# Kernel tuning notes

Measured on AMD Instinct MI355X. Metric: run time of the kernel, lower is better.

## Reference

```python
import jax, jax.numpy as jnp
import numpy as np

D_MODEL = 1024
N_HEADS = 16
D_K = D_MODEL // N_HEADS
D_FF = 4096
EPS = 1e-6


def setup_inputs() -> dict:
    key = jax.random.key(0)
    ks = jax.random.split(key, 12)
    s = 1.0 / np.sqrt(D_MODEL)
    inp = {
        "x": jax.random.normal(ks[0], (4, 2048, D_MODEL), jnp.float32),
        "src_mask": jnp.ones((4, 1, 1, 2048), jnp.int32),
        "Wq": jax.random.normal(ks[1], (D_MODEL, D_MODEL), jnp.float32) * s,
        "bq": jnp.zeros((D_MODEL,), jnp.float32),
        "Wk": jax.random.normal(ks[2], (D_MODEL, D_MODEL), jnp.float32) * s,
        "bk": jnp.zeros((D_MODEL,), jnp.float32),
        "Wv": jax.random.normal(ks[3], (D_MODEL, D_MODEL), jnp.float32) * s,
        "bv": jnp.zeros((D_MODEL,), jnp.float32),
        "Wo": jax.random.normal(ks[4], (D_MODEL, D_MODEL), jnp.float32) * s,
        "bo": jnp.zeros((D_MODEL,), jnp.float32),
        "W1": jax.random.normal(ks[5], (D_MODEL, D_FF), jnp.float32) * s,
        "b1": jnp.zeros((D_FF,), jnp.float32),
        "W2": jax.random.normal(ks[6], (D_FF, D_MODEL), jnp.float32) * (1.0 / np.sqrt(D_FF)),
        "b2": jnp.zeros((D_MODEL,), jnp.float32),
        # scalar LayerNormalization params (alpha=ones(1), bias=zeros(1)) for the 2 residual norms
        "ln1_alpha": jnp.ones((1,), jnp.float32),
        "ln1_bias": jnp.zeros((1,), jnp.float32),
        "ln2_alpha": jnp.ones((1,), jnp.float32),
        "ln2_bias": jnp.zeros((1,), jnp.float32),
    }
    return inp


def _layernorm(x, alpha, bias):
    # matches torch: mean + std (unbiased, ddof=1), (x-mean)/(std+eps)
    mean = jnp.mean(x, axis=-1, keepdims=True)
    std = jnp.std(x, axis=-1, keepdims=True, ddof=1)
    return alpha * ((x - mean) / (std + EPS)) + bias


def _mha(x, mask, Wq, bq, Wk, bk, Wv, bv, Wo, bo):
    B, S, _ = x.shape
    q = (x @ Wq + bq).reshape(B, S, N_HEADS, D_K).transpose(0, 2, 1, 3)
    k = (x @ Wk + bk).reshape(B, S, N_HEADS, D_K).transpose(0, 2, 1, 3)
    v = (x @ Wv + bv).reshape(B, S, N_HEADS, D_K).transpose(0, 2, 1, 3)
    scores = jnp.einsum("bhqd,bhkd->bhqk", q, k) / jnp.sqrt(jnp.float32(D_K))
    scores = jnp.where(mask == 0, jnp.float32(-1e9), scores)
    attn = jax.nn.softmax(scores, axis=-1)
    ctx = jnp.einsum("bhqk,bhkd->bhqd", attn, v)
    ctx = ctx.transpose(0, 2, 1, 3).reshape(B, S, D_MODEL)
    return ctx @ Wo + bo


def reference(x, src_mask, Wq, bq, Wk, bk, Wv, bv, Wo, bo, W1, b1, W2, b2,
              ln1_alpha, ln1_bias, ln2_alpha, ln2_bias):
    # pre-norm residual 1: self-attention
    h = _layernorm(x, ln1_alpha, ln1_bias)
    x = x + _mha(h, src_mask, Wq, bq, Wk, bk, Wv, bv, Wo, bo)
    # pre-norm residual 2: FFN
    h = _layernorm(x, ln2_alpha, ln2_bias)
    ff = jax.nn.relu(h @ W1 + b1) @ W2 + b2
    return x + ff
```

## Files before the change

### kernel.cpp

```cpp
#include <hip/hip_runtime.h>

typedef __attribute__((ext_vector_type(8))) short v8s;
typedef __attribute__((ext_vector_type(8))) unsigned short v8u;
typedef __attribute__((ext_vector_type(4))) unsigned short v4u;
typedef __attribute__((ext_vector_type(4))) float f32x4;

#define DEV __device__ __forceinline__

DEV unsigned short f2bf(float f) {
  union { float f; unsigned u; } v; v.f = f;
  unsigned r = v.u + 0x7fffu + ((v.u >> 16) & 1u);
  return (unsigned short)(r >> 16);
}

DEV float fexp2(float x) {
  float r; asm("v_exp_f32 %0, %1" : "=v"(r) : "v"(x)); return r;
}

DEV void gload16(const unsigned short* g, unsigned short* l) {
  __builtin_amdgcn_global_load_lds(
      (const __attribute__((address_space(1))) unsigned int*)g,
      (__attribute__((address_space(3))) unsigned int*)l, 16, 0, 0);
}

#define SL2E 0.1803368801111204f

__global__ __launch_bounds__(256) void ln_kernel(
    const float* __restrict__ x, unsigned short* __restrict__ h,
    const float* __restrict__ alpha, const float* __restrict__ beta)
{
  int row = blockIdx.x;
  int tid = threadIdx.x;
  const float4* xr = reinterpret_cast<const float4*>(x + (size_t)row * 1024);
  float4 v = xr[tid];
  float s  = v.x + v.y + v.z + v.w;
  float ss = v.x * v.x + v.y * v.y + v.z * v.z + v.w * v.w;
#pragma unroll
  for (int off = 1; off < 64; off <<= 1) {
    s  += __shfl_xor(s, off);
    ss += __shfl_xor(ss, off);
  }
  __shared__ float ps[4][2];
  int wid = tid >> 6, lane = tid & 63;
  if (lane == 0) { ps[wid][0] = s; ps[wid][1] = ss; }
  __syncthreads();
  s  = ps[0][0] + ps[1][0] + ps[2][0] + ps[3][0];
  ss = ps[0][1] + ps[1][1] + ps[2][1] + ps[3][1];
  float mean = s * (1.0f / 1024.0f);
  float var  = (ss - 1024.0f * mean * mean) * (1.0f / 1023.0f);
  float inv  = 1.0f / (sqrtf(fmaxf(var, 0.0f)) + 1e-6f);
  float a = alpha[0], b = beta[0];
  v4u o;
  o[0] = f2bf(a * ((v.x - mean) * inv) + b);
  o[1] = f2bf(a * ((v.y - mean) * inv) + b);
  o[2] = f2bf(a * ((v.z - mean) * inv) + b);
  o[3] = f2bf(a * ((v.w - mean) * inv) + b);
  *reinterpret_cast<v4u*>(h + (size_t)row * 1024 + tid * 4) = o;
}

__global__ __launch_bounds__(256) void transpose_convert(
    const float* __restrict__ W, unsigned short* __restrict__ Wt, int K, int N)
{
  __shared__ float t[32][33];
  int n0 = blockIdx.x * 32, k0 = blockIdx.y * 32;
  int tx = threadIdx.x, ty = threadIdx.y;
#pragma unroll
  for (int i = 0; i < 4; ++i)
    t[ty + i * 8][tx] = W[(size_t)(k0 + ty + i * 8) * N + n0 + tx];
  __syncthreads();
#pragma unroll
  for (int i = 0; i < 4; ++i)
    Wt[(size_t)(n0 + ty + i * 8) * K + k0 + tx] = f2bf(t[tx][ty + i * 8]);
}

enum { MODE_QKV = 0, MODE_RES = 2, MODE_FFN1 = 3 };

template <int MODE>
__global__ __launch_bounds__(512, 1) void gemm_256(
    const unsigned short* __restrict__ A, const unsigned short* __restrict__ Bt,
    const float* __restrict__ bias0, const float* __restrict__ bias1,
    const float* __restrict__ bias2,
    void* __restrict__ o0, void* __restrict__ o1, void* __restrict__ o2,
    int M, int N, int K)
{
  __shared__ unsigned short lds[2][512 * 64];

  int nbx = M >> 8, nwg = gridDim.x;
  int lin = blockIdx.x;
  int qq = nwg >> 3, rr = nwg & 7;
  int xcd = lin & 7, idx = lin >> 3;
  int swz = (xcd < rr ? xcd * (qq + 1) : rr * (qq + 1) + (xcd - rr) * qq) + idx;
  int bx = swz % nbx, by = swz / nbx;

  int tid = threadIdx.x, lane = tid & 63, wid = tid >> 6;
  int wm = wid >> 2, wn = wid & 3;
  int g = lane >> 4, c0 = lane & 15;
  int rowBase = bx * 256, colBase = by * 256;

  const unsigned short* Ab = A  + (size_t)rowBase * K;
  const unsigned short* Bb = Bt + (size_t)colBase * K;
  int NT = K >> 6;

  const unsigned short* src[8]; int dq[8];
#pragma unroll
  for (int i = 0; i < 8; ++i) {
    int q = i * 512 + tid;
    dq[i] = q;
    if (i < 4) {
      int r = q >> 3, p = q & 7;
      src[i] = Ab + (size_t)r * K + 8 * (p ^ (r & 7));
    } else {
      int qb2 = q - 2048, r = qb2 >> 3, p = qb2 & 7;
      src[i] = Bb + (size_t)r * K + 8 * (p ^ (r & 7));
    }
  }

  f32x4 acc[8][4];
#pragma unroll
  for (int m = 0; m < 8; ++m)
#pragma unroll
    for (int n = 0; n < 4; ++n) acc[m][n] = (f32x4){0.f, 0.f, 0.f, 0.f};

#define STG256(tt) do { \
    unsigned short* sb_ = &lds[(tt) & 1][0]; int ko_ = (tt) << 6; \
    _Pragma("unroll") for (int i = 0; i < 8; ++i) gload16(src[i] + ko_, sb_ + dq[i] * 8); \
  } while (0)

  STG256(0);
  asm volatile("s_waitcnt vmcnt(0)" ::: "memory");
  __builtin_amdgcn_s_barrier();
  asm volatile("" ::: "memory");

  for (int t = 0; t < NT; ++t) {
    const char* buf = (const char*)&lds[t & 1][0];
    bool more = (t + 1 < NT);
    if (more) STG256(t + 1);
    int e = (c0 & 7) << 4;

#pragma unroll
    for (int ph = 0; ph < 2; ++ph) {
      v8s af[8], bfr[4];
#pragma unroll
      for (int m = 0; m < 8; ++m) {
        int row = wm * 128 + m * 16 + c0;
        af[m] = *reinterpret_cast<const v8s*>(
            buf + row * 128 + ((ph * 64 + g * 16) ^ e));
      }
#pragma unroll
      for (int n = 0; n < 4; ++n) {
        int row = wn * 64 + n * 16 + c0;
        bfr[n] = *reinterpret_cast<const v8s*>(
            buf + 32768 + row * 128 + ((ph * 64 + g * 16) ^ e));
      }

      __builtin_amdgcn_s_setprio(1);
#pragma unroll
      for (int m = 0; m < 8; ++m)
#pragma unroll
        for (int n = 0; n < 4; ++n)
          acc[m][n] = __builtin_amdgcn_mfma_f32_16x16x32_bf16(
              af[m], bfr[n], acc[m][n], 0, 0, 0);
      __builtin_amdgcn_s_setprio(0);
    }

    if (more) asm volatile("s_waitcnt vmcnt(0)" ::: "memory");
    __builtin_amdgcn_sched_barrier(0);
    __builtin_amdgcn_s_barrier();
    asm volatile("" ::: "memory");
  }
#undef STG256

#pragma unroll
  for (int mf = 0; mf < 8; ++mf) {
#pragma unroll
    for (int nf = 0; nf < 4; ++nf) {
#pragma unroll
      for (int r = 0; r < 4; ++r) {
        int row = rowBase + wm * 128 + mf * 16 + g * 4 + r;
        int col = colBase + wn * 64 + nf * 16 + c0;
        float v = acc[mf][nf][r];
        if constexpr (MODE == MODE_QKV) {
          int sect = colBase >> 10;
          int cs = col & 1023;
          const float* bp = sect == 0 ? bias0 : (sect == 1 ? bias1 : bias2);
          v += bp[cs];
          int hh = cs >> 6, d = cs & 63;
          int b = row >> 11, sI = row & 2047;
          size_t bh = (size_t)(b * 16 + hh);
          if (sect == 0) {
            ((unsigned short*)o0)[(bh * 2048 + sI) * 64 + d] = f2bf(v * SL2E);
          } else if (sect == 1) {
            ((unsigned short*)o1)[(bh * 2048 + sI) * 64 + d] = f2bf(v);
          } else {
            int k6 = sI & 63;
            int slot = ((k6 >> 5) << 5) | (((k6 >> 2) & 3) << 3) |
                       (((k6 >> 4) & 1) << 2) | (k6 & 3);
            int e2 = slot ^ ((d & 7) << 3);
            ((unsigned short*)o2)[((bh * 32 + (sI >> 6)) * 64 + d) * 64 + e2] = f2bf(v);
          }
        } else {
          v += bias0[col];
          ((unsigned short*)o0)[(size_t)row * N + col] = f2bf(fmaxf(v, 0.0f));
        }
      }
    }
  }
}

#define BUF_ELEMS ((128 + 256) * 64)

DEV void stage_part(const unsigned short* Aptr, const unsigned short* Bptr,
                    unsigned short* buf, int K, int part, int wid, int lane)
{
  {
    int d = (part * 8 + wid) * 64 + lane;
    int r = d >> 3, p = d & 7;
    gload16(Aptr + (size_t)r * K + 8 * (p ^ (r & 7)),
            buf + (size_t)(part * 8 + wid) * 512);
  }
#pragma unroll
  for (int j = 0; j < 2; ++j) {
    int ib = part * 2 + j;
    int d = (ib * 8 + wid) * 64 + lane;
    int r = d >> 3, p = d & 7;
    gload16(Bptr + (size_t)r * K + 8 * (p ^ (r & 7)),
            buf + 128 * 64 + (size_t)(ib * 8 + wid) * 512);
  }
}

__global__ __launch_bounds__(512, 2) void gemm_pipe_res(
    const unsigned short* __restrict__ A, const unsigned short* __restrict__ Bt,
    const float* __restrict__ bias0, const float* __restrict__ resid,
    float* __restrict__ o0, int M, int N, int K)
{
  __shared__ unsigned short lds[3 * BUF_ELEMS];

  int nbx = M >> 7, nwg = gridDim.x;
  int lin = blockIdx.x;
  int qq = nwg >> 3, rr = nwg & 7;
  int xcd = lin & 7, idx = lin >> 3;
  int swz = (xcd < rr ? xcd * (qq + 1) : rr * (qq + 1) + (xcd - rr) * qq) + idx;
  int bx = swz % nbx, by = swz / nbx;

  int tid = threadIdx.x, lane = tid & 63, wid = tid >> 6;
  int wm = wid >> 2, wn = wid & 3;
  int g = lane >> 4, c0 = lane & 15;
  int rowBase = bx * 128, colBase = by * 256;

  const unsigned short* Ab = A  + (size_t)rowBase * K;
  const unsigned short* Bb = Bt + (size_t)colBase * K;
  int NT = K >> 6;

  f32x4 acc[4][4];
#pragma unroll
  for (int m = 0; m < 4; ++m)
#pragma unroll
    for (int n = 0; n < 4; ++n) acc[m][n] = (f32x4){0.f, 0.f, 0.f, 0.f};

  stage_part(Ab, Bb, lds, K, 0, wid, lane);
  stage_part(Ab, Bb, lds, K, 1, wid, lane);
  stage_part(Ab + 64, Bb + 64, lds + BUF_ELEMS, K, 0, wid, lane);
  stage_part(Ab + 64, Bb + 64, lds + BUF_ELEMS, K, 1, wid, lane);
  asm volatile("s_waitcnt vmcnt(6)" ::: "memory");
  __builtin_amdgcn_s_barrier();
  asm volatile("" ::: "memory");

  int cur = 0;
  for (int t = 0; t < NT; ++t) {
    const char* Abuf = (const char*)(lds + cur * BUF_ELEMS);
    const char* Bbuf = Abuf + 128 * 128;
    int nxt2 = cur + 2; if (nxt2 >= 3) nxt2 -= 3;
    unsigned short* sbuf = lds + nxt2 * BUF_ELEMS;
    bool doStage = (t + 2 < NT);
    int ks_ = (t + 2) << 6;
    int e = (c0 & 7) << 4;

#pragma unroll
    for (int ph = 0; ph < 2; ++ph) {
      v8s af[4], bfr[4];
#pragma unroll
      for (int m = 0; m < 4; ++m)
        af[m] = *reinterpret_cast<const v8s*>(
            Abuf + (wm * 64 + m * 16 + c0) * 128 + ((ph * 64 + g * 16) ^ e));
#pragma unroll
      for (int n = 0; n < 4; ++n)
        bfr[n] = *reinterpret_cast<const v8s*>(
            Bbuf + (wn * 64 + n * 16 + c0) * 128 + ((ph * 64 + g * 16) ^ e));

      if (doStage) stage_part(Ab + ks_, Bb + ks_, sbuf, K, ph, wid, lane);

      __builtin_amdgcn_s_setprio(1);
#pragma unroll
      for (int m = 0; m < 4; ++m)
#pragma unroll
        for (int n = 0; n < 4; ++n)
          acc[m][n] = __builtin_amdgcn_mfma_f32_16x16x32_bf16(
              af[m], bfr[n], acc[m][n], 0, 0, 0);
      __builtin_amdgcn_s_setprio(0);
    }

    if (doStage)            asm volatile("s_waitcnt vmcnt(6)" ::: "memory");
    else if (t + 1 < NT)    asm volatile("s_waitcnt vmcnt(0)" ::: "memory");
    __builtin_amdgcn_sched_barrier(0);
    __builtin_amdgcn_s_barrier();
    asm volatile("" ::: "memory");
    cur = cur + 1; if (cur >= 3) cur -= 3;
  }

#pragma unroll
  for (int mf = 0; mf < 4; ++mf) {
#pragma unroll
    for (int nf = 0; nf < 4; ++nf) {
#pragma unroll
      for (int r = 0; r < 4; ++r) {
        int row = rowBase + wm * 64 + mf * 16 + g * 4 + r;
        int col = colBase + wn * 64 + nf * 16 + c0;
        float v = acc[mf][nf][r] + bias0[col];
        o0[(size_t)row * N + col] = resid[(size_t)row * N + col] + v;
      }
    }
  }
}

__global__ __launch_bounds__(256) void attn_kernel(
    const unsigned short* __restrict__ q, const unsigned short* __restrict__ k,
    const unsigned short* __restrict__ vP, const int* __restrict__ mask,
    unsigned short* __restrict__ ctx)
{
  const int S = 2048, DK = 64, NT = 32;
  int bh = blockIdx.x;
  int b = bh >> 4, hh = bh & 15;
  int qbase = blockIdx.y * 128;
  int tid = threadIdx.x, lane = tid & 63, wid = tid >> 6;
  int g = lane >> 4, c0 = lane & 15;

  __shared__ unsigned short Ks[3 * 4096];
  __shared__ unsigned short Vs[3 * 4096];
  __shared__ unsigned short Mb[2048];

  const unsigned short* qb  = q  + (size_t)bh * S * DK;
  const unsigned short* kb  = k  + (size_t)bh * S * DK;
  const unsigned short* vPb = vP + (size_t)bh * 32 * 4096;
  const int* mb = mask + b * S;

  const int4* mb4 = reinterpret_cast<const int4*>(mb);
  int4 ma = mb4[tid * 2], mc = mb4[tid * 2 + 1];
  unsigned short bneg = f2bf(-1e9f);
  v8u bw;
  bw[0] = ma.x ? 0 : bneg; bw[1] = ma.y ? 0 : bneg;
  bw[2] = ma.z ? 0 : bneg; bw[3] = ma.w ? 0 : bneg;
  bw[4] = mc.x ? 0 : bneg; bw[5] = mc.y ? 0 : bneg;
  bw[6] = mc.z ? 0 : bneg; bw[7] = mc.w ? 0 : bneg;
  *reinterpret_cast<v8u*>(&Mb[tid * 8]) = bw;
  int ok = (ma.x && ma.y && ma.z && ma.w && mc.x && mc.y && mc.z && mc.w) ? 1 : 0;
  int allValid = __syncthreads_and(ok);

  int qrow = qbase + wid * 32 + c0;
  v8s aq[2][2];
#pragma unroll
  for (int s = 0; s < 2; ++s)
#pragma unroll
    for (int t = 0; t < 2; ++t)
      aq[s][t] = *reinterpret_cast<const v8s*>(
          &qb[(size_t)(qrow + s * 16) * DK + t * 32 + g * 8]);

  int i0 = tid, i1 = tid + 256;
  int r0 = i0 >> 3, m0 = i0 & 7;
  int r1 = i1 >> 3, m1 = i1 & 7;
  int ko0 = r0 * DK + 8 * (m0 ^ (r0 & 7));
  int ko1 = r1 * DK + 8 * (m1 ^ (r1 & 7));

  f32x4 acc[2][4];
#pragma unroll
  for (int s = 0; s < 2; ++s)
#pragma unroll
    for (int no = 0; no < 4; ++no) acc[s][no] = (f32x4){0.f, 0.f, 0.f, 0.f};
  float lsum0 = 0.f, lsum1 = 0.f;

#define ASTAGE(bi, tt) do { \
    int tb_ = (tt) * 4096; \
    gload16(kb + tb_ + ko0, Ks + (bi) * 4096 + i0 * 8); \
    gload16(kb + tb_ + ko1, Ks + (bi) * 4096 + i1 * 8); \
    gload16(vPb + tb_ + i0 * 8, Vs + (bi) * 4096 + i0 * 8); \
    gload16(vPb + tb_ + i1 * 8, Vs + (bi) * 4096 + i1 * 8); \
  } while (0)

  ASTAGE(0, 0);
  ASTAGE(1, 1);
  asm volatile("s_waitcnt vmcnt(4)" ::: "memory");
  __builtin_amdgcn_s_barrier();
  asm volatile("" ::: "memory");

  int cur = 0, nx2 = 2;
  for (int t = 0; t < NT; ++t) {
    bool more2 = (t + 2 < NT);
    if (more2) ASTAGE(nx2, t + 2);
    const unsigned short* Kc = Ks + cur * 4096;
    const unsigned short* Vc = Vs + cur * 4096;

    float p0[16], p1[16];
#pragma unroll
    for (int n = 0; n < 4; ++n) {
      int kvr = n * 16 + c0;
      const char* krow = (const char*)(Kc + kvr * DK);
      int sw = (kvr & 7) << 4;
      v8s ak0 = *reinterpret_cast<const v8s*>(krow + ((g * 16) ^ sw));
      v8s ak1 = *reinterpret_cast<const v8s*>(krow + ((64 + g * 16) ^ sw));
      f32x4 s0 = (f32x4){0.f, 0.f, 0.f, 0.f};
      f32x4 s1 = (f32x4){0.f, 0.f, 0.f, 0.f};
      s0 = __builtin_amdgcn_mfma_f32_16x16x32_bf16(ak0, aq[0][0], s0, 0, 0, 0);
      s0 = __builtin_amdgcn_mfma_f32_16x16x32_bf16(ak1, aq[0][1], s0, 0, 0, 0);
      s1 = __builtin_amdgcn_mfma_f32_16x16x32_bf16(ak0, aq[1][0], s1, 0, 0, 0);
      s1 = __builtin_amdgcn_mfma_f32_16x16x32_bf16(ak1, aq[1][1], s1, 0, 0, 0);
#pragma unroll
      for (int r = 0; r < 4; ++r) { p0[n * 4 + r] = s0[r]; p1[n * 4 + r] = s1[r]; }
    }
    if (!allValid) {
#pragma unroll
      for (int n = 0; n < 4; ++n) {
        v4u mbv = *reinterpret_cast<const v4u*>(&Mb[t * 64 + n * 16 + g * 4]);
#pragma unroll
        for (int r = 0; r < 4; ++r) {
          union { unsigned u; float f; } cv; cv.u = ((unsigned)mbv[r]) << 16;
          p0[n * 4 + r] += cv.f; p1[n * 4 + r] += cv.f;
        }
      }
    }

    float ts0 = 0.f, ts1 = 0.f;
#pragma unroll
    for (int i = 0; i < 16; ++i) {
      p0[i] = fexp2(p0[i]); ts0 += p0[i];
      p1[i] = fexp2(p1[i]); ts1 += p1[i];
    }
    lsum0 += ts0; lsum1 += ts1;

    v8s pb0[2], pb1[2];
#pragma unroll
    for (int c = 0; c < 2; ++c) {
      union { v8s s; unsigned u[4]; } k0, k1;
#pragma unroll
      for (int hp = 0; hp < 4; ++hp) {
        asm("v_cvt_pk_bf16_f32 %0, %1, %2"
            : "=v"(k0.u[hp]) : "v"(p0[c * 8 + 2 * hp]), "v"(p0[c * 8 + 2 * hp + 1]));
        asm("v_cvt_pk_bf16_f32 %0, %1, %2"
            : "=v"(k1.u[hp]) : "v"(p1[c * 8 + 2 * hp]), "v"(p1[c * 8 + 2 * hp + 1]));
      }
      pb0[c] = k0.s; pb1[c] = k1.s;
    }

#pragma unroll
    for (int c = 0; c < 2; ++c) {
#pragma unroll
      for (int no = 0; no < 4; ++no) {
        int d = no * 16 + c0;
        v8s av = *reinterpret_cast<const v8s*>(
            (const char*)(Vc + d * 64) + ((c * 64 + g * 16) ^ ((d & 7) << 4)));
        acc[0][no] = __builtin_amdgcn_mfma_f32_16x16x32_bf16(av, pb0[c], acc[0][no], 0, 0, 0);
        acc[1][no] = __builtin_amdgcn_mfma_f32_16x16x32_bf16(av, pb1[c], acc[1][no], 0, 0, 0);
      }
    }

    if (more2)              asm volatile("s_waitcnt vmcnt(4)" ::: "memory");
    else if (t + 1 < NT)    asm volatile("s_waitcnt vmcnt(0)" ::: "memory");
    __builtin_amdgcn_sched_barrier(0);
    __builtin_amdgcn_s_barrier();
    asm volatile("" ::: "memory");
    cur = (cur + 1 < 3) ? cur + 1 : 0;
    nx2 = (nx2 + 1 < 3) ? nx2 + 1 : 0;
  }
#undef ASTAGE

  lsum0 += __shfl_xor(lsum0, 16); lsum0 += __shfl_xor(lsum0, 32);
  lsum1 += __shfl_xor(lsum1, 16); lsum1 += __shfl_xor(lsum1, 32);
  float lrow[2] = {lsum0, lsum1};

#pragma unroll
  for (int s = 0; s < 2; ++s) {
    float inv = 1.0f / fmaxf(lrow[s], 1e-30f);
#pragma unroll
    for (int no = 0; no < 4; ++no) {
      v4u o;
      o[0] = f2bf(acc[s][no][0] * inv);
      o[1] = f2bf(acc[s][no][1] * inv);
      o[2] = f2bf(acc[s][no][2] * inv);
      o[3] = f2bf(acc[s][no][3] * inv);
      *reinterpret_cast<v4u*>(
          &ctx[(size_t)(b * S + qrow + s * 16) * 1024 + hh * 64 + no * 16 + g * 4]) = o;
    }
  }
}

extern "C" void kernel_launch(void* const* d_in, const int* in_sizes, int n_in,
                              void* d_out, int out_size, void* d_ws, size_t ws_size,
                              hipStream_t stream)
{
  (void)in_sizes; (void)n_in; (void)out_size; (void)ws_size;
  const float* x    = (const float*)d_in[0];
  const int*   mask = (const int*)d_in[1];
  const float* Wq = (const float*)d_in[2];  const float* bq = (const float*)d_in[3];
  const float* Wk = (const float*)d_in[4];  const float* bk = (const float*)d_in[5];
  const float* Wv = (const float*)d_in[6];  const float* bv = (const float*)d_in[7];
  const float* Wo = (const float*)d_in[8];  const float* bo = (const float*)d_in[9];
  const float* W1 = (const float*)d_in[10]; const float* b1 = (const float*)d_in[11];
  const float* W2 = (const float*)d_in[12]; const float* b2 = (const float*)d_in[13];
  const float* ln1a = (const float*)d_in[14]; const float* ln1b = (const float*)d_in[15];
  const float* ln2a = (const float*)d_in[16]; const float* ln2b = (const float*)d_in[17];

  char* ws = (char*)d_ws;
  const size_t MB = (size_t)1 << 20;
  unsigned short* wqkvT = (unsigned short*)(ws + 0 * MB);
  unsigned short* woT = (unsigned short*)(ws + 6 * MB);
  unsigned short* w1T = (unsigned short*)(ws + 8 * MB);
  unsigned short* w2T = (unsigned short*)(ws + 16 * MB);
  unsigned short* hb  = (unsigned short*)(ws + 24 * MB);
  unsigned short* qb  = (unsigned short*)(ws + 40 * MB);
  unsigned short* kb  = (unsigned short*)(ws + 56 * MB);
  unsigned short* vPb = (unsigned short*)(ws + 72 * MB);
  unsigned short* ctx = (unsigned short*)(ws + 88 * MB);
  unsigned short* gb  = (unsigned short*)(ws + 40 * MB);
  float* xout = (float*)d_out;

  dim3 tb(32, 8);
  transpose_convert<<<dim3(32, 32),  tb, 0, stream>>>(Wq, wqkvT,               1024, 1024);
  transpose_convert<<<dim3(32, 32),  tb, 0, stream>>>(Wk, wqkvT + 1024 * 1024, 1024, 1024);
  transpose_convert<<<dim3(32, 32),  tb, 0, stream>>>(Wv, wqkvT + 2048 * 1024, 1024, 1024);
  transpose_convert<<<dim3(32, 32),  tb, 0, stream>>>(Wo, woT, 1024, 1024);
  transpose_convert<<<dim3(128, 32), tb, 0, stream>>>(W1, w1T, 1024, 4096);
  transpose_convert<<<dim3(32, 128), tb, 0, stream>>>(W2, w2T, 4096, 1024);

  ln_kernel<<<8192, 256, 0, stream>>>(x, hb, ln1a, ln1b);

  gemm_256<MODE_QKV><<<384, 512, 0, stream>>>(
      hb, wqkvT, bq, bk, bv, qb, kb, vPb, 8192, 3072, 1024);

  attn_kernel<<<dim3(64, 16), 256, 0, stream>>>(qb, kb, vPb, mask, ctx);

  gemm_pipe_res<<<256, 512, 0, stream>>>(ctx, woT, bo, x, xout, 8192, 1024, 1024);

  ln_kernel<<<8192, 256, 0, stream>>>(xout, hb, ln2a, ln2b);

  gemm_256<MODE_FFN1><<<512, 512, 0, stream>>>(
      hb, w1T, b1, nullptr, nullptr, gb, nullptr, nullptr, 8192, 4096, 1024);

  gemm_pipe_res<<<256, 512, 0, stream>>>(gb, w2T, b2, xout, xout, 8192, 1024, 4096);
}
```

Before: 401.4 us.

## Unify GEMMs into triple-buffered 256x128 kernel and widen attention per-wave query tile

Replaces the double-buffered 256x256 GEMM and the 128x256 residual GEMM with one 256x128 triple-buffered kernel (two workgroups per CU) that stages two K-tiles ahead and splits A/B staging across the two MFMA phases. The attention kernel now handles 64 query rows per wave (256 per block) and gets its softmax row sums from an MFMA against a ones vector instead of scalar adds and shuffles. The aim is better latency hiding and occupancy in the GEMMs, and more reuse of K/V tiles in attention. The costs are higher register pressure in attention and fewer attention workgroups in flight.

Result: slower. 413.9 us (+3.1%).

```diff
diff --git a/kernel.cpp b/kernel.cpp
--- a/kernel.cpp
+++ b/kernel.cpp
@@ -75,15 +75,17 @@
 
 enum { MODE_QKV = 0, MODE_RES = 2, MODE_FFN1 = 3 };
 
+#define WBUF_E ((256 + 128) * 64)
+
 template <int MODE>
-__global__ __launch_bounds__(512, 1) void gemm_256(
+__global__ __launch_bounds__(512, 2) void gemm_wide(
     const unsigned short* __restrict__ A, const unsigned short* __restrict__ Bt,
     const float* __restrict__ bias0, const float* __restrict__ bias1,
-    const float* __restrict__ bias2,
+    const float* __restrict__ bias2, const float* __restrict__ resid,
     void* __restrict__ o0, void* __restrict__ o1, void* __restrict__ o2,
     int M, int N, int K)
 {
-  __shared__ unsigned short lds[2][512 * 64];
+  __shared__ unsigned short lds[3 * WBUF_E];
 
   int nbx = M >> 8, nwg = gridDim.x;
   int lin = blockIdx.x;
@@ -95,89 +97,101 @@
   int tid = threadIdx.x, lane = tid & 63, wid = tid >> 6;
   int wm = wid >> 2, wn = wid & 3;
   int g = lane >> 4, c0 = lane & 15;
-  int rowBase = bx * 256, colBase = by * 256;
+  int rowBase = bx * 256, colBase = by * 128;
 
   const unsigned short* Ab = A  + (size_t)rowBase * K;
   const unsigned short* Bb = Bt + (size_t)colBase * K;
   int NT = K >> 6;
 
-  const unsigned short* src[8]; int dq[8];
-#pragma unroll
-  for (int i = 0; i < 8; ++i) {
-    int q = i * 512 + tid;
-    dq[i] = q;
-    if (i < 4) {
-      int r = q >> 3, p = q & 7;
-      src[i] = Ab + (size_t)r * K + 8 * (p ^ (r & 7));
-    } else {
-      int qb2 = q - 2048, r = qb2 >> 3, p = qb2 & 7;
-      src[i] = Bb + (size_t)r * K + 8 * (p ^ (r & 7));
-    }
-  }
-
-  f32x4 acc[8][4];
+  const unsigned short* srcA[4]; int dqA[4];
+  const unsigned short* srcB[2]; int dqB[2];
+#pragma unroll
+  for (int c = 0; c < 4; ++c) {
+    int d = c * 512 + tid, r = d >> 3, p = d & 7;
+    srcA[c] = Ab + (size_t)r * K + 8 * (p ^ (r & 7));
+    dqA[c] = d;
+  }
+#pragma unroll
+  for (int c = 0; c < 2; ++c) {
+    int d = c * 512 + tid, r = d >> 3, p = d & 7;
+    srcB[c] = Bb + (size_t)r * K + 8 * (p ^ (r & 7));
+    dqB[c] = d;
+  }
+
+  f32x4 acc[8][2];
 #pragma unroll
   for (int m = 0; m < 8; ++m)
 #pragma unroll
-    for (int n = 0; n < 4; ++n) acc[m][n] = (f32x4){0.f, 0.f, 0.f, 0.f};
-
-#define STG256(tt) do { \
-    unsigned short* sb_ = &lds[(tt) & 1][0]; int ko_ = (tt) << 6; \
-    _Pragma("unroll") for (int i = 0; i < 8; ++i) gload16(src[i] + ko_, sb_ + dq[i] * 8); \
+    for (int n = 0; n < 2; ++n) acc[m][n] = (f32x4){0.f, 0.f, 0.f, 0.f};
+
+#define WSTAGE_A(bi, tt) do { \
+    unsigned short* sb_ = lds + (bi) * WBUF_E; int ko_ = (tt) << 6; \
+    _Pragma("unroll") for (int c = 0; c < 4; ++c) gload16(srcA[c] + ko_, sb_ + dqA[c] * 8); \
   } while (0)
-
-  STG256(0);
-  asm volatile("s_waitcnt vmcnt(0)" ::: "memory");
+#define WSTAGE_B(bi, tt) do { \
+    unsigned short* sb_ = lds + (bi) * WBUF_E + 256 * 64; int ko_ = (tt) << 6; \
+    _Pragma("unroll") for (int c = 0; c < 2; ++c) gload16(srcB[c] + ko_, sb_ + dqB[c] * 8); \
+  } while (0)
+
+  WSTAGE_A(0, 0); WSTAGE_B(0, 0);
+  WSTAGE_A(1, 1); WSTAGE_B(1, 1);
+  asm volatile("s_waitcnt vmcnt(6)" ::: "memory");
   __builtin_amdgcn_s_barrier();
   asm volatile("" ::: "memory");
 
+  int cur = 0;
   for (int t = 0; t < NT; ++t) {
-    const char* buf = (const char*)&lds[t & 1][0];
-    bool more = (t + 1 < NT);
-    if (more) STG256(t + 1);
-    int e = (c0 & 7) << 4;
+    const char* Abuf = (const char*)(lds + cur * WBUF_E);
+    const char* Bbuf = Abuf + 256 * 128;
+    int nxt2 = cur + 2; if (nxt2 >= 3) nxt2 -= 3;
+    bool doStage = (t + 2 < NT);
 
 #pragma unroll
     for (int ph = 0; ph < 2; ++ph) {
-      v8s af[8], bfr[4];
+      v8s af[8], bfr[2];
 #pragma unroll
       for (int m = 0; m < 8; ++m) {
         int row = wm * 128 + m * 16 + c0;
         af[m] = *reinterpret_cast<const v8s*>(
-            buf + row * 128 + ((ph * 64 + g * 16) ^ e));
-      }
-#pragma unroll
-      for (int n = 0; n < 4; ++n) {
-        int row = wn * 64 + n * 16 + c0;
+            Abuf + row * 128 + ((ph * 64 + g * 16) ^ ((row & 7) << 4)));
+      }
+#pragma unroll
+      for (int n = 0; n < 2; ++n) {
+        int row = wn * 32 + n * 16 + c0;
         bfr[n] = *reinterpret_cast<const v8s*>(
-            buf + 32768 + row * 128 + ((ph * 64 + g * 16) ^ e));
-      }
+            Bbuf + row * 128 + ((ph * 64 + g * 16) ^ ((row & 7) << 4)));
+      }
+
+      if (doStage) { if (ph == 0) WSTAGE_A(nxt2, t + 2); else WSTAGE_B(nxt2, t + 2); }
 
       __builtin_amdgcn_s_setprio(1);
 #pragma unroll
       for (int m = 0; m < 8; ++m)
 #pragma unroll
-        for (int n = 0; n < 4; ++n)
+        for (int n = 0; n < 2; ++n)
           acc[m][n] = __builtin_amdgcn_mfma_f32_16x16x32_bf16(
               af[m], bfr[n], acc[m][n], 0, 0, 0);
       __builtin_amdgcn_s_setprio(0);
     }
 
-    if (more) asm volatile("s_waitcnt vmcnt(0)" ::: "memory");
+    if (doStage)            asm volatile("s_waitcnt vmcnt(6)" ::: "memory");
+    else if (t + 1 < NT)    asm volatile("s_waitcnt vmcnt(0)" ::: "memory");
     __builtin_amdgcn_sched_barrier(0);
     __builtin_amdgcn_s_barrier();
     asm volatile("" ::: "memory");
-  }
-#undef STG256
+    cur = cur + 1; if (cur >= 3) cur -= 3;
+  }
+#undef WSTAGE_A
+#undef WSTAGE_B
 
 #pragma unroll
   for (int mf = 0; mf < 8; ++mf) {
 #pragma unroll
-    for (int nf = 0; nf < 4; ++nf) {
+    for (int nf = 0; nf < 2; ++nf) {
 #pragma unroll
       for (int r = 0; r < 4; ++r) {
         int row = rowBase + wm * 128 + mf * 16 + g * 4 + r;
-        int col = colBase + wn * 64 + nf * 16 + c0;
+        int col = colBase + wn * 32 + nf * 16 + c0;
         float v = acc[mf][nf][r];
         if constexpr (MODE == MODE_QKV) {
           int sect = colBase >> 10;
@@ -198,6 +212,10 @@
             int e2 = slot ^ ((d & 7) << 3);
             ((unsigned short*)o2)[((bh * 32 + (sI >> 6)) * 64 + d) * 64 + e2] = f2bf(v);
           }
+        } else if constexpr (MODE == MODE_RES) {
+          v += bias0[col];
+          ((float*)o0)[(size_t)row * N + col] =
+              resid[(size_t)row * N + col] + v;
         } else {
           v += bias0[col];
           ((unsigned short*)o0)[(size_t)row * N + col] = f2bf(fmaxf(v, 0.0f));
@@ -207,122 +225,7 @@
   }
 }
 
-#define BUF_ELEMS ((128 + 256) * 64)
-
-DEV void stage_part(const unsigned short* Aptr, const unsigned short* Bptr,
-                    unsigned short* buf, int K, int part, int wid, int lane)
-{
-  {
-    int d = (part * 8 + wid) * 64 + lane;
-    int r = d >> 3, p = d & 7;
-    gload16(Aptr + (size_t)r * K + 8 * (p ^ (r & 7)),
-            buf + (size_t)(part * 8 + wid) * 512);
-  }
-#pragma unroll
-  for (int j = 0; j < 2; ++j) {
-    int ib = part * 2 + j;
-    int d = (ib * 8 + wid) * 64 + lane;
-    int r = d >> 3, p = d & 7;
-    gload16(Bptr + (size_t)r * K + 8 * (p ^ (r & 7)),
-            buf + 128 * 64 + (size_t)(ib * 8 + wid) * 512);
-  }
-}
-
-__global__ __launch_bounds__(512, 2) void gemm_pipe_res(
-    const unsigned short* __restrict__ A, const unsigned short* __restrict__ Bt,
-    const float* __restrict__ bias0, const float* __restrict__ resid,
-    float* __restrict__ o0, int M, int N, int K)
-{
-  __shared__ unsigned short lds[3 * BUF_ELEMS];
-
-  int nbx = M >> 7, nwg = gridDim.x;
-  int lin = blockIdx.x;
-  int qq = nwg >> 3, rr = nwg & 7;
-  int xcd = lin & 7, idx = lin >> 3;
-  int swz = (xcd < rr ? xcd * (qq + 1) : rr * (qq + 1) + (xcd - rr) * qq) + idx;
-  int bx = swz % nbx, by = swz / nbx;
-
-  int tid = threadIdx.x, lane = tid & 63, wid = tid >> 6;
-  int wm = wid >> 2, wn = wid & 3;
-  int g = lane >> 4, c0 = lane & 15;
-  int rowBase = bx * 128, colBase = by * 256;
-
-  const unsigned short* Ab = A  + (size_t)rowBase * K;
-  const unsigned short* Bb = Bt + (size_t)colBase * K;
-  int NT = K >> 6;
-
-  f32x4 acc[4][4];
-#pragma unroll
-  for (int m = 0; m < 4; ++m)
-#pragma unroll
-    for (int n = 0; n < 4; ++n) acc[m][n] = (f32x4){0.f, 0.f, 0.f, 0.f};
-
-  stage_part(Ab, Bb, lds, K, 0, wid, lane);
-  stage_part(Ab, Bb, lds, K, 1, wid, lane);
-  stage_part(Ab + 64, Bb + 64, lds + BUF_ELEMS, K, 0, wid, lane);
-  stage_part(Ab + 64, Bb + 64, lds + BUF_ELEMS, K, 1, wid, lane);
-  asm volatile("s_waitcnt vmcnt(6)" ::: "memory");
-  __builtin_amdgcn_s_barrier();
-  asm volatile("" ::: "memory");
-
-  int cur = 0;
-  for (int t = 0; t < NT; ++t) {
-    const char* Abuf = (const char*)(lds + cur * BUF_ELEMS);
-    const char* Bbuf = Abuf + 128 * 128;
-    int nxt2 = cur + 2; if (nxt2 >= 3) nxt2 -= 3;
-    unsigned short* sbuf = lds + nxt2 * BUF_ELEMS;
-    bool doStage = (t + 2 < NT);
-    int ks_ = (t + 2) << 6;
-    int e = (c0 & 7) << 4;
-
-#pragma unroll
-    for (int ph = 0; ph < 2; ++ph) {
-      v8s af[4], bfr[4];
-#pragma unroll
-      for (int m = 0; m < 4; ++m)
-        af[m] = *reinterpret_cast<const v8s*>(
-            Abuf + (wm * 64 + m * 16 + c0) * 128 + ((ph * 64 + g * 16) ^ e));
-#pragma unroll
-      for (int n = 0; n < 4; ++n)
-        bfr[n] = *reinterpret_cast<const v8s*>(
-            Bbuf + (wn * 64 + n * 16 + c0) * 128 + ((ph * 64 + g * 16) ^ e));
-
-      if (doStage) stage_part(Ab + ks_, Bb + ks_, sbuf, K, ph, wid, lane);
-
-      __builtin_amdgcn_s_setprio(1);
-#pragma unroll
-      for (int m = 0; m < 4; ++m)
-#pragma unroll
-        for (int n = 0; n < 4; ++n)
-          acc[m][n] = __builtin_amdgcn_mfma_f32_16x16x32_bf16(
-              af[m], bfr[n], acc[m][n], 0, 0, 0);
-      __builtin_amdgcn_s_setprio(0);
-    }
-
-    if (doStage)            asm volatile("s_waitcnt vmcnt(6)" ::: "memory");
-    else if (t + 1 < NT)    asm volatile("s_waitcnt vmcnt(0)" ::: "memory");
-    __builtin_amdgcn_sched_barrier(0);
-    __builtin_amdgcn_s_barrier();
-    asm volatile("" ::: "memory");
-    cur = cur + 1; if (cur >= 3) cur -= 3;
-  }
-
-#pragma unroll
-  for (int mf = 0; mf < 4; ++mf) {
-#pragma unroll
-    for (int nf = 0; nf < 4; ++nf) {
-#pragma unroll
-      for (int r = 0; r < 4; ++r) {
-        int row = rowBase + wm * 64 + mf * 16 + g * 4 + r;
-        int col = colBase + wn * 64 + nf * 16 + c0;
-        float v = acc[mf][nf][r] + bias0[col];
-        o0[(size_t)row * N + col] = resid[(size_t)row * N + col] + v;
-      }
-    }
-  }
-}
-
-__global__ __launch_bounds__(256) void attn_kernel(
+__global__ __launch_bounds__(256, 2) void attn_kernel(
     const unsigned short* __restrict__ q, const unsigned short* __restrict__ k,
     const unsigned short* __restrict__ vP, const int* __restrict__ mask,
     unsigned short* __restrict__ ctx)
@@ -330,7 +233,7 @@
   const int S = 2048, DK = 64, NT = 32;
   int bh = blockIdx.x;
   int b = bh >> 4, hh = bh & 15;
-  int qbase = blockIdx.y * 128;
+  int qbase = blockIdx.y * 256;
   int tid = threadIdx.x, lane = tid & 63, wid = tid >> 6;
   int g = lane >> 4, c0 = lane & 15;
 
@@ -352,13 +255,13 @@
   bw[4] = mc.x ? 0 : bneg; bw[5] = mc.y ? 0 : bneg;
   bw[6] = mc.z ? 0 : bneg; bw[7] = mc.w ? 0 : bneg;
   *reinterpret_cast<v8u*>(&Mb[tid * 8]) = bw;
-  int ok = (ma.x && ma.y && ma.z && ma.w && mc.x && mc.y && mc.z && mc.w) ? 1 : 0;
-  int allValid = __syncthreads_and(ok);
-
-  int qrow = qbase + wid * 32 + c0;
-  v8s aq[2][2];
-#pragma unroll
-  for (int s = 0; s < 2; ++s)
+  int okm = (ma.x && ma.y && ma.z && ma.w && mc.x && mc.y && mc.z && mc.w) ? 1 : 0;
+  int allValid = __syncthreads_and(okm);
+
+  int qrow = qbase + wid * 64 + c0;
+  v8s aq[4][2];
+#pragma unroll
+  for (int s = 0; s < 4; ++s)
 #pragma unroll
     for (int t = 0; t < 2; ++t)
       aq[s][t] = *reinterpret_cast<const v8s*>(
@@ -370,12 +273,16 @@
   int ko0 = r0 * DK + 8 * (m0 ^ (r0 & 7));
   int ko1 = r1 * DK + 8 * (m1 ^ (r1 & 7));
 
-  f32x4 acc[2][4];
-#pragma unroll
-  for (int s = 0; s < 2; ++s)
+  f32x4 acc[4][4], accl[4];
+#pragma unroll
+  for (int s = 0; s < 4; ++s) {
+    accl[s] = (f32x4){0.f, 0.f, 0.f, 0.f};
 #pragma unroll
     for (int no = 0; no < 4; ++no) acc[s][no] = (f32x4){0.f, 0.f, 0.f, 0.f};
-  float lsum0 = 0.f, lsum1 = 0.f;
+  }
+  v8s ones;
+#pragma unroll
+  for (int j = 0; j < 8; ++j) ones[j] = (short)0x3F80;
 
 #define ASTAGE(bi, tt) do { \
     int tb_ = (tt) * 4096; \
@@ -398,57 +305,54 @@
     const unsigned short* Kc = Ks + cur * 4096;
     const unsigned short* Vc = Vs + cur * 4096;
 
-    float p0[16], p1[16];
-#pragma unroll
-    for (int n = 0; n < 4; ++n) {
-      int kvr = n * 16 + c0;
-      const char* krow = (const char*)(Kc + kvr * DK);
-      int sw = (kvr & 7) << 4;
-      v8s ak0 = *reinterpret_cast<const v8s*>(krow + ((g * 16) ^ sw));
-      v8s ak1 = *reinterpret_cast<const v8s*>(krow + ((64 + g * 16) ^ sw));
-      f32x4 s0 = (f32x4){0.f, 0.f, 0.f, 0.f};
-      f32x4 s1 = (f32x4){0.f, 0.f, 0.f, 0.f};
-      s0 = __builtin_amdgcn_mfma_f32_16x16x32_bf16(ak0, aq[0][0], s0, 0, 0, 0);
-      s0 = __builtin_amdgcn_mfma_f32_16x16x32_bf16(ak1, aq[0][1], s0, 0, 0, 0);
-      s1 = __builtin_amdgcn_mfma_f32_16x16x32_bf16(ak0, aq[1][0], s1, 0, 0, 0);
-      s1 = __builtin_amdgcn_mfma_f32_16x16x32_bf16(ak1, aq[1][1], s1, 0, 0, 0);
-#pragma unroll
-      for (int r = 0; r < 4; ++r) { p0[n * 4 + r] = s0[r]; p1[n * 4 + r] = s1[r]; }
+    v8s pb[4][2];
+#pragma unroll
+    for (int pp = 0; pp < 2; ++pp) {
+      float pA[16], pB[16];
+#pragma unroll
+      for (int n = 0; n < 4; ++n) {
+        int kvr = n * 16 + c0;
+        const char* krow = (const char*)(Kc + kvr * DK);
+        int sw = (kvr & 7) << 4;
+        v8s ak0 = *reinterpret_cast<const v8s*>(krow + ((g * 16) ^ sw));
+        v8s ak1 = *reinterpret_cast<const v8s*>(krow + ((64 + g * 16) ^ sw));
+        f32x4 s0 = (f32x4){0.f, 0.f, 0.f, 0.f};
+        f32x4 s1 = (f32x4){0.f, 0.f, 0.f, 0.f};
+        s0 = __builtin_amdgcn_mfma_f32_16x16x32_bf16(ak0, aq[pp * 2][0], s0, 0, 0, 0);
+        s0 = __builtin_amdgcn_mfma_f32_16x16x32_bf16(ak1, aq[pp * 2][1], s0, 0, 0, 0);
+        s1 = __builtin_amdgcn_mfma_f32_16x16x32_bf16(ak0, aq[pp * 2 + 1][0], s1, 0, 0, 0);
+        s1 = __builtin_amdgcn_mfma_f32_16x16x32_bf16(ak1, aq[pp * 2 + 1][1], s1, 0, 0, 0);
+#pragma unroll
+        for (int r = 0; r < 4; ++r) { pA[n * 4 + r] = s0[r]; pB[n * 4 + r] = s1[r]; }
+      }
+      if (!allValid) {
+#pragma unroll
+        for (int n = 0; n < 4; ++n) {
+          v4u mbv = *reinterpret_cast<const v4u*>(&Mb[t * 64 + n * 16 + g * 4]);
+#pragma unroll
+          for (int r = 0; r < 4; ++r) {
+            union { unsigned u; float f; } cv; cv.u = ((unsigned)mbv[r]) << 16;
+            pA[n * 4 + r] += cv.f; pB[n * 4 + r] += cv.f;
+          }
+        }
+      }
+#pragma unroll
+      for (int i = 0; i < 16; ++i) { pA[i] = fexp2(pA[i]); pB[i] = fexp2(pB[i]); }
+#pragma unroll
+      for (int c = 0; c < 2; ++c) {
+        union { v8s s; unsigned u[4]; } kA, kB;
+#pragma unroll
+        for (int hp = 0; hp < 4; ++hp) {
+          asm("v_cvt_pk_bf16_f32 %0, %1, %2"
+              : "=v"(kA.u[hp]) : "v"(pA[c * 8 + 2 * hp]), "v"(pA[c * 8 + 2 * hp + 1]));
+          asm("v_cvt_pk_bf16_f32 %0, %1, %2"
+              : "=v"(kB.u[hp]) : "v"(pB[c * 8 + 2 * hp]), "v"(pB[c * 8 + 2 * hp + 1]));
+        }
+        pb[pp * 2][c] = kA.s; pb[pp * 2 + 1][c] = kB.s;
+      }
     }
-    if (!allValid) {
-#pragma unroll
-      for (int n = 0; n < 4; ++n) {
-        v4u mbv = *reinterpret_cast<const v4u*>(&Mb[t * 64 + n * 16 + g * 4]);
-#pragma unroll
-        for (int r = 0; r < 4; ++r) {
-          union { unsigned u; float f; } cv; cv.u = ((unsigned)mbv[r]) << 16;
-          p0[n * 4 + r] += cv.f; p1[n * 4 + r] += cv.f;
-        }
-      }
-    }
-
-    float ts0 = 0.f, ts1 = 0.f;
-#pragma unroll
-    for (int i = 0; i < 16; ++i) {
-      p0[i] = fexp2(p0[i]); ts0 += p0[i];
-      p1[i] = fexp2(p1[i]); ts1 += p1[i];
-    }
-    lsum0 += ts0; lsum1 += ts1;
-
-    v8s pb0[2], pb1[2];
-#pragma unroll
-    for (int c = 0; c < 2; ++c) {
-      union { v8s s; unsigned u[4]; } k0, k1;
-#pragma unroll
-      for (int hp = 0; hp < 4; ++hp) {
-        asm("v_cvt_pk_bf16_f32 %0, %1, %2"
-            : "=v"(k0.u[hp]) : "v"(p0[c * 8 + 2 * hp]), "v"(p0[c * 8 + 2 * hp + 1]));
-        asm("v_cvt_pk_bf16_f32 %0, %1, %2"
-            : "=v"(k1.u[hp]) : "v"(p1[c * 8 + 2 * hp]), "v"(p1[c * 8 + 2 * hp + 1]));
-      }
-      pb0[c] = k0.s; pb1[c] = k1.s;
-    }
-
+
+    __builtin_amdgcn_s_setprio(1);
 #pragma unroll
     for (int c = 0; c < 2; ++c) {
 #pragma unroll
@@ -456,10 +360,15 @@
         int d = no * 16 + c0;
         v8s av = *reinterpret_cast<const v8s*>(
             (const char*)(Vc + d * 64) + ((c * 64 + g * 16) ^ ((d & 7) << 4)));
-        acc[0][no] = __builtin_amdgcn_mfma_f32_16x16x32_bf16(av, pb0[c], acc[0][no], 0, 0, 0);
-        acc[1][no] = __builtin_amdgcn_mfma_f32_16x16x32_bf16(av, pb1[c], acc[1][no], 0, 0, 0);
-      }
+#pragma unroll
+        for (int s = 0; s < 4; ++s)
+          acc[s][no] = __builtin_amdgcn_mfma_f32_16x16x32_bf16(av, pb[s][c], acc[s][no], 0, 0, 0);
+      }
+#pragma unroll
+      for (int s = 0; s < 4; ++s)
+        accl[s] = __builtin_amdgcn_mfma_f32_16x16x32_bf16(ones, pb[s][c], accl[s], 0, 0, 0);
     }
+    __builtin_amdgcn_s_setprio(0);
 
     if (more2)              asm volatile("s_waitcnt vmcnt(4)" ::: "memory");
     else if (t + 1 < NT)    asm volatile("s_waitcnt vmcnt(0)" ::: "memory");
@@ -471,13 +380,9 @@
   }
 #undef ASTAGE
 
-  lsum0 += __shfl_xor(lsum0, 16); lsum0 += __shfl_xor(lsum0, 32);
-  lsum1 += __shfl_xor(lsum1, 16); lsum1 += __shfl_xor(lsum1, 32);
-  float lrow[2] = {lsum0, lsum1};
-
-#pragma unroll
-  for (int s = 0; s < 2; ++s) {
-    float inv = 1.0f / fmaxf(lrow[s], 1e-30f);
+#pragma unroll
+  for (int s = 0; s < 4; ++s) {
+    float inv = 1.0f / fmaxf(accl[s][0], 1e-30f);
 #pragma unroll
     for (int no = 0; no < 4; ++no) {
       v4u o;
@@ -531,17 +436,19 @@
 
   ln_kernel<<<8192, 256, 0, stream>>>(x, hb, ln1a, ln1b);
 
-  gemm_256<MODE_QKV><<<384, 512, 0, stream>>>(
-      hb, wqkvT, bq, bk, bv, qb, kb, vPb, 8192, 3072, 1024);
-
-  attn_kernel<<<dim3(64, 16), 256, 0, stream>>>(qb, kb, vPb, mask, ctx);
-
-  gemm_pipe_res<<<256, 512, 0, stream>>>(ctx, woT, bo, x, xout, 8192, 1024, 1024);
+  gemm_wide<MODE_QKV><<<768, 512, 0, stream>>>(
+      hb, wqkvT, bq, bk, bv, nullptr, qb, kb, vPb, 8192, 3072, 1024);
+
+  attn_kernel<<<dim3(64, 8), 256, 0, stream>>>(qb, kb, vPb, mask, ctx);
+
+  gemm_wide<MODE_RES><<<256, 512, 0, stream>>>(
+      ctx, woT, bo, nullptr, nullptr, x, xout, nullptr, nullptr, 8192, 1024, 1024);
 
   ln_kernel<<<8192, 256, 0, stream>>>(xout, hb, ln2a, ln2b);
 
-  gemm_256<MODE_FFN1><<<512, 512, 0, stream>>>(
-      hb, w1T, b1, nullptr, nullptr, gb, nullptr, nullptr, 8192, 4096, 1024);
-
-  gemm_pipe_res<<<256, 512, 0, stream>>>(gb, w2T, b2, xout, xout, 8192, 1024, 4096);
-}
+  gemm_wide<MODE_FFN1><<<1024, 512, 0, stream>>>(
+      hb, w1T, b1, nullptr, nullptr, nullptr, gb, nullptr, nullptr, 8192, 4096, 1024);
+
+  gemm_wide<MODE_RES><<<256, 512, 0, stream>>>(
+      gb, w2T, b2, nullptr, nullptr, xout, xout, nullptr, nullptr, 8192, 1024, 4096);
+}
```
